# Optimization experiments

Hardware: AMD Instinct MI355X
Metric: run time of the kernel (lower is better)

Reference implementation:

```python
import jax, jax.numpy as jnp
import numpy as np

EPS = 1e-6

def _rmsnorm(x, w):
    # fp32 RMSNorm over last dim
    var = jnp.mean(x * x, axis=-1, keepdims=True)
    return w * (x * jax.lax.rsqrt(var + EPS))

def setup_inputs() -> dict:
    key = jax.random.key(0)
    ks = jax.random.split(key, 6)
    S, D, H = 4096, 1024, 16
    HD = D // H
    return {
        "hidden_states": jax.random.normal(ks[0], (S, D), jnp.float32),
        "qkv_w": jax.random.normal(ks[1], (3 * D, D), jnp.float32) * 0.02,
        "qkv_b": jnp.zeros((3 * D,), jnp.float32),
        "proj_w": jax.random.normal(ks[2], (D, D), jnp.float32) * 0.02,
        "proj_b": jnp.zeros((D,), jnp.float32),
        "q_norm_w": jnp.ones((D,), jnp.float32),
        "k_norm_w": jnp.ones((D,), jnp.float32),
        "rotary_freqs": jax.random.normal(ks[3], (S, HD // 2), jnp.float32),
        "cu_seqlens": jnp.array([0, 1024, 2048, 3072, 4096], jnp.int32),
        "num_heads": 16,
    }

def reference(hidden_states, qkv_w, qkv_b, proj_w, proj_b, q_norm_w, k_norm_w, rotary_freqs, cu_seqlens, num_heads):
    S, D = hidden_states.shape
    H = num_heads
    hd = D // H
    # QKV projection
    qkv = hidden_states @ qkv_w.T + qkv_b           # [S, 3D]
    qkv = qkv.reshape(S, 3, H, hd)
    q, k, v = qkv[:, 0], qkv[:, 1], qkv[:, 2]       # each [S, H, hd]
    # QK RMSNorm over the flattened hidden dim (InternVL style)
    q = _rmsnorm(q.reshape(S, D), q_norm_w).reshape(S, H, hd)
    k = _rmsnorm(k.reshape(S, D), k_norm_w).reshape(S, H, hd)
    # RoPE: freqs [S, hd/2] -> cos/sin [S, 1, hd] (tiled, not interleaved)
    cos = jnp.cos(rotary_freqs)
    sin = jnp.sin(rotary_freqs)
    cos = jnp.concatenate([cos, cos], axis=-1)[:, None, :]
    sin = jnp.concatenate([sin, sin], axis=-1)[:, None, :]
    def rope(t):
        x1, x2 = jnp.split(t, 2, axis=-1)
        rot = jnp.concatenate([-x2, x1], axis=-1)
        return t * cos + rot * sin
    q = rope(q)
    k = rope(k)
    # Block-diagonal mask from cu_seqlens: same-segment tokens attend
    seg = jnp.searchsorted(cu_seqlens[1:], jnp.arange(S), side='right')  # [S]
    mask = seg[:, None] == seg[None, :]                                   # [S, S]
    scale = 1.0 / jnp.sqrt(jnp.float32(hd))
    scores = jnp.einsum('shd,thd->hst', q, k) * scale                     # [H, S, S]
    scores = jnp.where(mask[None], scores, jnp.float32(-1e30))
    probs = jax.nn.softmax(scores, axis=-1)
    out = jnp.einsum('hst,thd->shd', probs, v).reshape(S, D)
    return out @ proj_w.T + proj_b
```

## Files before the change

kernel.cpp:

```cpp
#include <hip/hip_runtime.h>
#include <hip/hip_bf16.h>

#define S 4096
#define D 1024
#define NH 16
#define HD 64

typedef float f32x4 __attribute__((ext_vector_type(4)));
typedef __bf16 bf16x8 __attribute__((ext_vector_type(8)));

#define MFMA16(a, b, c) __builtin_amdgcn_mfma_f32_16x16x32_bf16((a), (b), (c), 0, 0, 0)

__device__ __forceinline__ unsigned short f2bf(float f) {
  unsigned int u = __builtin_bit_cast(unsigned int, f);
  u += 0x7FFFu + ((u >> 16) & 1u);
  return (unsigned short)(u >> 16);
}

__device__ __forceinline__ float bf2f(unsigned short u) {
  unsigned int x = ((unsigned int)u) << 16;
  return __builtin_bit_cast(float, x);
}

__device__ __forceinline__ unsigned cvtpk(float lo, float hi) {
  unsigned r;
  asm("v_cvt_pk_bf16_f32 %0, %1, %2" : "=v"(r) : "v"(lo), "v"(hi));
  return r;
}

typedef __attribute__((address_space(1))) void GAS;
typedef __attribute__((address_space(3))) void LAS;

__device__ __forceinline__ void gld_lds16(const unsigned short* g, unsigned short* l) {
  __builtin_amdgcn_global_load_lds((GAS*)g, (LAS*)l, 16, 0, 0);
}

__global__ void cvt3(const float* __restrict__ a, unsigned short* __restrict__ ao,
                     const float* __restrict__ b, unsigned short* __restrict__ bo,
                     const float* __restrict__ c, unsigned short* __restrict__ co) {
  int i = blockIdx.x * blockDim.x + threadIdx.x;
  const float* in;
  unsigned short* out;
  int j;
  if (i < 1048576) { in = a; out = ao; j = i; }
  else if (i < 1835008) { in = b; out = bo; j = i - 1048576; }
  else { in = c; out = co; j = i - 1835008; }
  float4 v = ((const float4*)in)[j];
  ushort4 u;
  u.x = f2bf(v.x); u.y = f2bf(v.y); u.z = f2bf(v.z); u.w = f2bf(v.w);
  ((ushort4*)out)[j] = u;
}

__device__ __forceinline__ int xcd_swz(int bid, int nwg) {
  int q = nwg >> 3;
  return (bid & 7) * q + (bid >> 3);
}

#define GSTEP(RA, RB, SA, SB, KN, COND)                                           \
  {                                                                               \
    bf16x8 af[4], bfv[4];                                                         \
    _Pragma("unroll") for (int mf = 0; mf < 4; ++mf)                              \
        af[mf] = *(const bf16x8*)&RA[(wr * 64 + mf * 16 + l15) * 32 + l4 * 8];    \
    _Pragma("unroll") for (int nf = 0; nf < 4; ++nf)                              \
        bfv[nf] = *(const bf16x8*)&RB[(wc * 64 + nf * 16 + l15) * 32 + l4 * 8];   \
    if (COND) {                                                                   \
      gld_lds16(Ab + (size_t)r0 * K + (KN) + o0, &SA[w * 512]);                   \
      gld_lds16(Ab + (size_t)r1 * K + (KN) + o1, &SA[2048 + w * 512]);            \
      gld_lds16(Bb + (size_t)r0 * K + (KN) + o0, &SB[w * 512]);                   \
      gld_lds16(Bb + (size_t)r1 * K + (KN) + o1, &SB[2048 + w * 512]);            \
    }                                                                             \
    _Pragma("unroll") for (int mf = 0; mf < 4; ++mf)                              \
        _Pragma("unroll") for (int nf = 0; nf < 4; ++nf)                          \
            acc[mf][nf] = MFMA16(af[mf], bfv[nf], acc[mf][nf]);                   \
    __syncthreads();                                                              \
  }

__global__ __launch_bounds__(256) void gemm_qkv(const unsigned short* __restrict__ A,
                                                const unsigned short* __restrict__ B,
                                                const float* __restrict__ bias,
                                                unsigned short* __restrict__ qk,
                                                unsigned short* __restrict__ vt) {
  __shared__ __align__(16) unsigned short As0[4096], As1[4096];
  __shared__ __align__(16) unsigned short Bs0[4096], Bs1[4096];
  __shared__ __align__(16) unsigned short tr[128 * 65];
  const int K = 1024;
  const int t = threadIdx.x;
  const int lane = t & 63;
  const int w = t >> 6;
  const int wr = w >> 1, wc = w & 1;
  const int l15 = lane & 15, l4 = lane >> 4;
  const int bid = blockIdx.y * 24 + blockIdx.x;
  const int r8 = bid & 7, i = bid >> 3;
  const int by = (r8 >> 1) * 8 + i / 12;
  const int bx = (r8 & 1) * 12 + i % 12;
  const int m0 = by * 128, n0 = bx * 128;

  f32x4 acc[4][4] = {};

  const int r0 = t >> 2, o0 = (t & 3) * 8;
  const int r1 = (256 + t) >> 2, o1 = ((256 + t) & 3) * 8;
  const unsigned short* Ab = A + (size_t)m0 * K;
  const unsigned short* Bb = B + (size_t)n0 * K;

  gld_lds16(Ab + (size_t)r0 * K + o0, &As0[w * 512]);
  gld_lds16(Ab + (size_t)r1 * K + o1, &As0[2048 + w * 512]);
  gld_lds16(Bb + (size_t)r0 * K + o0, &Bs0[w * 512]);
  gld_lds16(Bb + (size_t)r1 * K + o1, &Bs0[2048 + w * 512]);
  __syncthreads();

#pragma unroll 1
  for (int k0 = 0; k0 < K; k0 += 64) {
    GSTEP(As0, Bs0, As1, Bs1, k0 + 32, true);
    GSTEP(As1, Bs1, As0, Bs0, k0 + 64, k0 + 64 < K);
  }

  if (n0 < 2048) {
#pragma unroll
    for (int mf = 0; mf < 4; ++mf)
#pragma unroll
      for (int nf = 0; nf < 4; ++nf) {
        int rr = m0 + wr * 64 + mf * 16 + l4 * 4;
        int cc = n0 + wc * 64 + nf * 16 + l15;
        float bv = bias[cc];
#pragma unroll
        for (int j = 0; j < 4; ++j)
          qk[(size_t)(rr + j) * 2048 + cc] = f2bf(acc[mf][nf][j] + bv);
      }
  } else {
    const int h0 = (n0 - 2048) >> 6;
#pragma unroll
    for (int p = 0; p < 2; ++p) {
      if (wc == p) {
#pragma unroll
        for (int mf = 0; mf < 4; ++mf)
#pragma unroll
          for (int nf = 0; nf < 4; ++nf) {
            int srow = wr * 64 + mf * 16 + l4 * 4;
            int cl = nf * 16 + l15;
            float bv = bias[n0 + p * 64 + cl];
#pragma unroll
            for (int j = 0; j < 4; ++j)
              tr[(srow + j) * 65 + cl] = f2bf(acc[mf][nf][j] + bv);
          }
      }
      __syncthreads();
      const int hh = h0 + p;
#pragma unroll
      for (int i2 = 0; i2 < 8; ++i2) {
        int idx = i2 * 256 + t;
        int d = idx >> 5, sc = idx & 31;
        ushort4 u;
        u.x = tr[(sc * 4 + 0) * 65 + d];
        u.y = tr[(sc * 4 + 1) * 65 + d];
        u.z = tr[(sc * 4 + 2) * 65 + d];
        u.w = tr[(sc * 4 + 3) * 65 + d];
        *(ushort4*)(vt + (size_t)hh * HD * S + (size_t)d * S + m0 + sc * 4) = u;
      }
      __syncthreads();
    }
  }
}

__global__ __launch_bounds__(256) void gemm_bt(const unsigned short* __restrict__ A,
                                               const unsigned short* __restrict__ B,
                                               const float* __restrict__ bias,
                                               float* __restrict__ C,
                                               int M, int N, int K, int gx) {
  __shared__ __align__(16) unsigned short As0[4096], As1[4096];
  __shared__ __align__(16) unsigned short Bs0[4096], Bs1[4096];
  const int t = threadIdx.x;
  const int lane = t & 63;
  const int w = t >> 6;
  const int wr = w >> 1, wc = w & 1;
  const int l15 = lane & 15, l4 = lane >> 4;
  const int nwg = gridDim.x * gridDim.y;
  const int nbid = xcd_swz(blockIdx.y * gx + blockIdx.x, nwg);
  const int m0 = (nbid / gx) * 128, n0 = (nbid % gx) * 128;

  f32x4 acc[4][4] = {};

  const int r0 = t >> 2, o0 = (t & 3) * 8;
  const int r1 = (256 + t) >> 2, o1 = ((256 + t) & 3) * 8;
  const unsigned short* Ab = A + (size_t)m0 * K;
  const unsigned short* Bb = B + (size_t)n0 * K;

  gld_lds16(Ab + (size_t)r0 * K + o0, &As0[w * 512]);
  gld_lds16(Ab + (size_t)r1 * K + o1, &As0[2048 + w * 512]);
  gld_lds16(Bb + (size_t)r0 * K + o0, &Bs0[w * 512]);
  gld_lds16(Bb + (size_t)r1 * K + o1, &Bs0[2048 + w * 512]);
  __syncthreads();

#pragma unroll 1
  for (int k0 = 0; k0 < K; k0 += 64) {
    GSTEP(As0, Bs0, As1, Bs1, k0 + 32, true);
    GSTEP(As1, Bs1, As0, Bs0, k0 + 64, k0 + 64 < K);
  }

#pragma unroll
  for (int mf = 0; mf < 4; ++mf) {
#pragma unroll
    for (int nf = 0; nf < 4; ++nf) {
      int rr = m0 + wr * 64 + mf * 16 + l4 * 4;
      int cc = n0 + wc * 64 + nf * 16 + l15;
      float bv = bias[cc];
#pragma unroll
      for (int j = 0; j < 4; ++j)
        C[(size_t)(rr + j) * N + cc] = acc[mf][nf][j] + bv;
    }
  }
}

__global__ __launch_bounds__(256) void norm_rope(const unsigned short* __restrict__ qk,
                                                 const float* __restrict__ qw,
                                                 const float* __restrict__ kw,
                                                 const float* __restrict__ fr,
                                                 unsigned short* __restrict__ qo,
                                                 unsigned short* __restrict__ ko) {
  __shared__ float buf[1024];
  __shared__ float red[4];
  const int s = blockIdx.x, t = threadIdx.x;
  const int lane = t & 63, w = t >> 6;
  const int e = t * 4;
  const int hh = e >> 6, dd = e & 63;
  const float* frow = fr + (size_t)s * 32;
  float cs[4], sn[4];
#pragma unroll
  for (int i = 0; i < 4; ++i) {
    float f = frow[(dd + i) & 31];
    cs[i] = cosf(f);
    sn[i] = sinf(f);
  }
  for (int part = 0; part < 2; ++part) {
    const unsigned short* row = qk + (size_t)s * 2048 + part * 1024;
    const float* wvp = part ? kw : qw;
    unsigned short* op = part ? ko : qo;
    const float oscale = part ? 1.0f : 0.18033688011112042f;
    ushort4 uv = *(const ushort4*)(row + e);
    float vx = bf2f(uv.x), vy = bf2f(uv.y), vz = bf2f(uv.z), vw = bf2f(uv.w);
    float ssq = vx * vx + vy * vy + vz * vz + vw * vw;
#pragma unroll
    for (int off = 1; off < 64; off <<= 1) ssq += __shfl_xor(ssq, off, 64);
    if (part) __syncthreads();
    if (lane == 0) red[w] = ssq;
    __syncthreads();
    float inv = rsqrtf((red[0] + red[1] + red[2] + red[3]) * (1.0f / 1024.0f) + 1e-6f);
    float4 wv = *(const float4*)(wvp + e);
    buf[e + 0] = vx * inv * wv.x;
    buf[e + 1] = vy * inv * wv.y;
    buf[e + 2] = vz * inv * wv.z;
    buf[e + 3] = vw * inv * wv.w;
    __syncthreads();
    unsigned short ov[4];
#pragma unroll
    for (int i = 0; i < 4; ++i) {
      int di = dd + i;
      float x = buf[e + i];
      float rot = (di < 32) ? -buf[e + i + 32] : buf[e + i - 32];
      ov[i] = f2bf((x * cs[i] + rot * sn[i]) * oscale);
    }
    unsigned short* dst = op + (size_t)hh * S * HD + (size_t)s * HD + dd;
    dst[0] = ov[0]; dst[1] = ov[1]; dst[2] = ov[2]; dst[3] = ov[3];
  }
}

__device__ __forceinline__ void qk_tile(f32x4* s4, const unsigned short* Kbuf,
                                        bf16x8 qf0, bf16x8 qf1, int l15, int l4) {
#pragma unroll
  for (int nf = 0; nf < 4; ++nf) {
    const int row = nf * 16 + l15;
    const int roff = row * 64;
    const int sw = (row & 7) << 3;
    bf16x8 k0 = *(const bf16x8*)&Kbuf[roff + ((l4 * 8) ^ sw)];
    bf16x8 k1 = *(const bf16x8*)&Kbuf[roff + ((32 + l4 * 8) ^ sw)];
    s4[nf] = MFMA16(k0, qf0, s4[nf]);
    s4[nf] = MFMA16(k1, qf1, s4[nf]);
  }
}

__global__ __launch_bounds__(256) void attn_kernel(const unsigned short* __restrict__ q,
                                                   const unsigned short* __restrict__ k,
                                                   const unsigned short* __restrict__ vt,
                                                   unsigned short* __restrict__ aout) {
  __shared__ __align__(16) unsigned short Ks[2][4096];
  __shared__ __align__(16) unsigned short Vs[3][4096];
  const int bid = blockIdx.x;
  const int xcd = bid & 7;
  const int idx = bid >> 3;
  const int gw = idx >> 4, qt = idx & 15;
  const int g = xcd * 8 + gw;
  const int h = g >> 2, seg = g & 3;
  const int t = threadIdx.x, lane = t & 63, w = t >> 6;
  const int l15 = lane & 15, l4 = lane >> 4;
  const size_t hb = (size_t)h * S * HD;
  const int q0 = seg * 1024 + qt * 64 + w * 16;
  const int kvbase = seg * 1024;

  const int sr = t >> 3;
  const int scb = (t & 7) ^ (sr & 7);
  const unsigned short* ksrcA = k + hb + (size_t)(kvbase + sr) * HD + scb * 8;
  const unsigned short* ksrcB = ksrcA + 32 * HD;
  const unsigned short* vsrcA = vt + (size_t)h * HD * S + (size_t)sr * S + kvbase + scb * 8;
  const unsigned short* vsrcB = vsrcA + (size_t)32 * S;

  const unsigned short* qp = q + hb + (size_t)(q0 + l15) * HD + l4 * 8;
  bf16x8 qf0 = *(const bf16x8*)qp;
  bf16x8 qf1 = *(const bf16x8*)(qp + 32);

  f32x4 o[4] = {};
  float m = -1e30f, l = 0.f;

  gld_lds16(ksrcA, &Ks[0][w * 512]);
  gld_lds16(ksrcB, &Ks[0][2048 + w * 512]);
  gld_lds16(ksrcA + 4096, &Ks[1][w * 512]);
  gld_lds16(ksrcB + 4096, &Ks[1][2048 + w * 512]);
  gld_lds16(vsrcA, &Vs[0][w * 512]);
  gld_lds16(vsrcB, &Vs[0][2048 + w * 512]);
  gld_lds16(vsrcA + 64, &Vs[1][w * 512]);
  gld_lds16(vsrcB + 64, &Vs[1][2048 + w * 512]);
  __syncthreads();

  f32x4 cur[4] = {};
  qk_tile(cur, Ks[0], qf0, qf1, l15, l4);
  __syncthreads();

#pragma unroll
  for (int it = 0; it < 16; ++it) {
    if (it < 14) {
      gld_lds16(ksrcA + (it + 2) * 4096, &Ks[it & 1][w * 512]);
      gld_lds16(ksrcB + (it + 2) * 4096, &Ks[it & 1][2048 + w * 512]);
      gld_lds16(vsrcA + (it + 2) * 64, &Vs[(it + 2) % 3][w * 512]);
      gld_lds16(vsrcB + (it + 2) * 64, &Vs[(it + 2) % 3][2048 + w * 512]);
    }
    f32x4 nxt[4] = {};
    if (it < 15) {
      __builtin_amdgcn_s_setprio(1);
      qk_tile(nxt, Ks[(it + 1) & 1], qf0, qf1, l15, l4);
      __builtin_amdgcn_s_setprio(0);
      __builtin_amdgcn_sched_barrier(0);
    }
    float t0 = fmaxf(fmaxf(cur[0][0], cur[0][1]), cur[0][2]);
    float t1 = fmaxf(fmaxf(cur[0][3], cur[1][0]), cur[1][1]);
    float t2 = fmaxf(fmaxf(cur[1][2], cur[1][3]), cur[2][0]);
    float t3 = fmaxf(fmaxf(cur[2][1], cur[2][2]), cur[2][3]);
    float t4 = fmaxf(fmaxf(cur[3][0], cur[3][1]), cur[3][2]);
    float lmax = fmaxf(fmaxf(fmaxf(t0, t1), fmaxf(t2, t3)), fmaxf(t4, cur[3][3]));
    if (!__all(lmax <= m + 8.0f)) {
      float tmax = fmaxf(lmax, __shfl_xor(lmax, 16, 64));
      tmax = fmaxf(tmax, __shfl_xor(tmax, 32, 64));
      const float mn = fmaxf(m, tmax);
      const float corr = exp2f(m - mn);
      m = mn;
      l *= corr;
#pragma unroll
      for (int nf2 = 0; nf2 < 4; ++nf2)
#pragma unroll
        for (int j = 0; j < 4; ++j) o[nf2][j] *= corr;
    }
    float p[4][4];
#pragma unroll
    for (int nf = 0; nf < 4; ++nf)
#pragma unroll
      for (int j = 0; j < 4; ++j) {
        float e = exp2f(cur[nf][j] - m);
        p[nf][j] = e;
        l += e;
      }
    unsigned pk[4][2];
#pragma unroll
    for (int nf = 0; nf < 4; ++nf) {
      pk[nf][0] = cvtpk(p[nf][0], p[nf][1]);
      pk[nf][1] = cvtpk(p[nf][2], p[nf][3]);
    }
    const int srcbase = ((lane >> 4) & 1) * 32 + l15;
    const bool hi = (lane & 32) != 0;
    const unsigned short* Vbuf = Vs[it % 3];
#pragma unroll
    for (int ks = 0; ks < 2; ++ks) {
      unsigned bw[4];
#pragma unroll
      for (int h2 = 0; h2 < 2; ++h2)
#pragma unroll
        for (int r = 0; r < 2; ++r) {
          unsigned E = (unsigned)__shfl((int)pk[2 * ks][r], srcbase + h2 * 16, 64);
          unsigned F = (unsigned)__shfl((int)pk[2 * ks + 1][r], srcbase + h2 * 16, 64);
          bw[h2 * 2 + r] = hi ? F : E;
        }
      bf16x8 pb = __builtin_bit_cast(bf16x8, *(uint4*)bw);
      __builtin_amdgcn_s_setprio(1);
#pragma unroll
      for (int nf2 = 0; nf2 < 4; ++nf2) {
        const int row = nf2 * 16 + l15;
        const int roff = row * 64;
        const int sw = (row & 7) << 3;
        bf16x8 vf = *(const bf16x8*)&Vbuf[roff + ((ks * 32 + l4 * 8) ^ sw)];
        o[nf2] = MFMA16(vf, pb, o[nf2]);
      }
      __builtin_amdgcn_s_setprio(0);
    }
    __syncthreads();
    cur[0] = nxt[0]; cur[1] = nxt[1]; cur[2] = nxt[2]; cur[3] = nxt[3];
  }

  l += __shfl_xor(l, 16, 64);
  l += __shfl_xor(l, 32, 64);
  const float invl = 1.0f / l;
#pragma unroll
  for (int nf2 = 0; nf2 < 4; ++nf2) {
    ushort4 u;
    u.x = f2bf(o[nf2][0] * invl);
    u.y = f2bf(o[nf2][1] * invl);
    u.z = f2bf(o[nf2][2] * invl);
    u.w = f2bf(o[nf2][3] * invl);
    *(ushort4*)(aout + (size_t)(q0 + l15) * D + h * 64 + nf2 * 16 + l4 * 4) = u;
  }
}

extern "C" void kernel_launch(void* const* d_in, const int* in_sizes, int n_in,
                              void* d_out, int out_size, void* d_ws, size_t ws_size,
                              hipStream_t stream) {
  const float* hidden = (const float*)d_in[0];
  const float* qkvw   = (const float*)d_in[1];
  const float* qkvb   = (const float*)d_in[2];
  const float* projw  = (const float*)d_in[3];
  const float* projb  = (const float*)d_in[4];
  const float* qnw    = (const float*)d_in[5];
  const float* knw    = (const float*)d_in[6];
  const float* freqs  = (const float*)d_in[7];
  float* out = (float*)d_out;
  char* ws = (char*)d_ws;

  unsigned short* hb  = (unsigned short*)(ws + 0);
  unsigned short* wb  = (unsigned short*)(ws + (8u << 20));
  unsigned short* pb  = (unsigned short*)(ws + (14u << 20));
  unsigned short* qk  = (unsigned short*)(ws + (16u << 20));
  unsigned short* vtb = (unsigned short*)(ws + (32u << 20));
  unsigned short* qb  = (unsigned short*)(ws + (40u << 20));
  unsigned short* kb  = (unsigned short*)(ws + (48u << 20));
  unsigned short* ab  = (unsigned short*)(ws + (56u << 20));

  cvt3<<<8192, 256, 0, stream>>>(hidden, hb, qkvw, wb, projw, pb);
  gemm_qkv<<<dim3(24, 32), 256, 0, stream>>>(hb, wb, qkvb, qk, vtb);
  norm_rope<<<4096, 256, 0, stream>>>(qk, qnw, knw, freqs, qb, kb);
  attn_kernel<<<1024, 256, 0, stream>>>(qb, kb, vtb, ab);
  gemm_bt<<<dim3(8, 32), 256, 0, stream>>>(ab, pb, projb, out, 4096, 1024, 1024, 8);
}
```

Before: 133.4 us.

## Process two 16-row query groups per wave in attention to reuse K/V tiles

Each wave now handles 32 query rows (two 16-row groups) instead of 16. Each K and V fragment read from LDS feeds two MFMAs, and each block covers 128 queries, so the grid drops from 1024 to 512 blocks. This halves global K/V tile loads and LDS fragment reads per query. The cost is more accumulator and score registers, which may lower occupancy, and fewer blocks to spread across CUs.

```diff
diff --git a/kernel.cpp b/kernel.cpp
--- a/kernel.cpp
+++ b/kernel.cpp
@@ -263,8 +263,9 @@
   }
 }
 
-__device__ __forceinline__ void qk_tile(f32x4* s4, const unsigned short* Kbuf,
-                                        bf16x8 qf0, bf16x8 qf1, int l15, int l4) {
+__device__ __forceinline__ void qk_tile2(f32x4* sA, f32x4* sB, const unsigned short* Kbuf,
+                                         bf16x8 qA0, bf16x8 qA1, bf16x8 qB0, bf16x8 qB1,
+                                         int l15, int l4) {
 #pragma unroll
   for (int nf = 0; nf < 4; ++nf) {
     const int row = nf * 16 + l15;
@@ -272,8 +273,10 @@
     const int sw = (row & 7) << 3;
     bf16x8 k0 = *(const bf16x8*)&Kbuf[roff + ((l4 * 8) ^ sw)];
     bf16x8 k1 = *(const bf16x8*)&Kbuf[roff + ((32 + l4 * 8) ^ sw)];
-    s4[nf] = MFMA16(k0, qf0, s4[nf]);
-    s4[nf] = MFMA16(k1, qf1, s4[nf]);
+    sA[nf] = MFMA16(k0, qA0, sA[nf]);
+    sA[nf] = MFMA16(k1, qA1, sA[nf]);
+    sB[nf] = MFMA16(k0, qB0, sB[nf]);
+    sB[nf] = MFMA16(k1, qB1, sB[nf]);
   }
 }
 
@@ -286,13 +289,13 @@
   const int bid = blockIdx.x;
   const int xcd = bid & 7;
   const int idx = bid >> 3;
-  const int gw = idx >> 4, qt = idx & 15;
+  const int gw = idx >> 3, qt = idx & 7;
   const int g = xcd * 8 + gw;
   const int h = g >> 2, seg = g & 3;
   const int t = threadIdx.x, lane = t & 63, w = t >> 6;
   const int l15 = lane & 15, l4 = lane >> 4;
   const size_t hb = (size_t)h * S * HD;
-  const int q0 = seg * 1024 + qt * 64 + w * 16;
+  const int q0 = seg * 1024 + qt * 128 + w * 32;
   const int kvbase = seg * 1024;
 
   const int sr = t >> 3;
@@ -302,12 +305,15 @@
   const unsigned short* vsrcA = vt + (size_t)h * HD * S + (size_t)sr * S + kvbase + scb * 8;
   const unsigned short* vsrcB = vsrcA + (size_t)32 * S;
 
-  const unsigned short* qp = q + hb + (size_t)(q0 + l15) * HD + l4 * 8;
-  bf16x8 qf0 = *(const bf16x8*)qp;
-  bf16x8 qf1 = *(const bf16x8*)(qp + 32);
-
-  f32x4 o[4] = {};
-  float m = -1e30f, l = 0.f;
+  const unsigned short* qpA = q + hb + (size_t)(q0 + l15) * HD + l4 * 8;
+  const unsigned short* qpB = q + hb + (size_t)(q0 + 16 + l15) * HD + l4 * 8;
+  bf16x8 qA0 = *(const bf16x8*)qpA;
+  bf16x8 qA1 = *(const bf16x8*)(qpA + 32);
+  bf16x8 qB0 = *(const bf16x8*)qpB;
+  bf16x8 qB1 = *(const bf16x8*)(qpB + 32);
+
+  f32x4 oA[4] = {}, oB[4] = {};
+  float mA = -1e30f, lA = 0.f, mB = -1e30f, lB = 0.f;
 
   gld_lds16(ksrcA, &Ks[0][w * 512]);
   gld_lds16(ksrcB, &Ks[0][2048 + w * 512]);
@@ -319,8 +325,8 @@
   gld_lds16(vsrcB + 64, &Vs[1][2048 + w * 512]);
   __syncthreads();
 
-  f32x4 cur[4] = {};
-  qk_tile(cur, Ks[0], qf0, qf1, l15, l4);
+  f32x4 curA[4] = {}, curB[4] = {};
+  qk_tile2(curA, curB, Ks[0], qA0, qA1, qB0, qB1, l15, l4);
   __syncthreads();
 
 #pragma unroll
@@ -331,61 +337,73 @@
       gld_lds16(vsrcA + (it + 2) * 64, &Vs[(it + 2) % 3][w * 512]);
       gld_lds16(vsrcB + (it + 2) * 64, &Vs[(it + 2) % 3][2048 + w * 512]);
     }
-    f32x4 nxt[4] = {};
+    f32x4 nxtA[4] = {}, nxtB[4] = {};
     if (it < 15) {
       __builtin_amdgcn_s_setprio(1);
-      qk_tile(nxt, Ks[(it + 1) & 1], qf0, qf1, l15, l4);
+      qk_tile2(nxtA, nxtB, Ks[(it + 1) & 1], qA0, qA1, qB0, qB1, l15, l4);
       __builtin_amdgcn_s_setprio(0);
       __builtin_amdgcn_sched_barrier(0);
     }
-    float t0 = fmaxf(fmaxf(cur[0][0], cur[0][1]), cur[0][2]);
-    float t1 = fmaxf(fmaxf(cur[0][3], cur[1][0]), cur[1][1]);
-    float t2 = fmaxf(fmaxf(cur[1][2], cur[1][3]), cur[2][0]);
-    float t3 = fmaxf(fmaxf(cur[2][1], cur[2][2]), cur[2][3]);
-    float t4 = fmaxf(fmaxf(cur[3][0], cur[3][1]), cur[3][2]);
-    float lmax = fmaxf(fmaxf(fmaxf(t0, t1), fmaxf(t2, t3)), fmaxf(t4, cur[3][3]));
-    if (!__all(lmax <= m + 8.0f)) {
-      float tmax = fmaxf(lmax, __shfl_xor(lmax, 16, 64));
-      tmax = fmaxf(tmax, __shfl_xor(tmax, 32, 64));
-      const float mn = fmaxf(m, tmax);
-      const float corr = exp2f(m - mn);
-      m = mn;
-      l *= corr;
-#pragma unroll
-      for (int nf2 = 0; nf2 < 4; ++nf2)
-#pragma unroll
-        for (int j = 0; j < 4; ++j) o[nf2][j] *= corr;
-    }
-    float p[4][4];
-#pragma unroll
-    for (int nf = 0; nf < 4; ++nf)
-#pragma unroll
-      for (int j = 0; j < 4; ++j) {
-        float e = exp2f(cur[nf][j] - m);
-        p[nf][j] = e;
-        l += e;
-      }
-    unsigned pk[4][2];
-#pragma unroll
-    for (int nf = 0; nf < 4; ++nf) {
-      pk[nf][0] = cvtpk(p[nf][0], p[nf][1]);
-      pk[nf][1] = cvtpk(p[nf][2], p[nf][3]);
+    unsigned pkA[4][2], pkB[4][2];
+#pragma unroll
+    for (int gq = 0; gq < 2; ++gq) {
+      f32x4* cur = gq ? curB : curA;
+      float& m = gq ? mB : mA;
+      float& l = gq ? lB : lA;
+      f32x4* o = gq ? oB : oA;
+      unsigned(*pk)[2] = gq ? pkB : pkA;
+      float t0 = fmaxf(fmaxf(cur[0][0], cur[0][1]), cur[0][2]);
+      float t1 = fmaxf(fmaxf(cur[0][3], cur[1][0]), cur[1][1]);
+      float t2 = fmaxf(fmaxf(cur[1][2], cur[1][3]), cur[2][0]);
+      float t3 = fmaxf(fmaxf(cur[2][1], cur[2][2]), cur[2][3]);
+      float t4 = fmaxf(fmaxf(cur[3][0], cur[3][1]), cur[3][2]);
+      float lmax = fmaxf(fmaxf(fmaxf(t0, t1), fmaxf(t2, t3)), fmaxf(t4, cur[3][3]));
+      if (!__all(lmax <= m + 8.0f)) {
+        float tmax = fmaxf(lmax, __shfl_xor(lmax, 16, 64));
+        tmax = fmaxf(tmax, __shfl_xor(tmax, 32, 64));
+        const float mn = fmaxf(m, tmax);
+        const float corr = exp2f(m - mn);
+        m = mn;
+        l *= corr;
+#pragma unroll
+        for (int nf2 = 0; nf2 < 4; ++nf2)
+#pragma unroll
+          for (int j = 0; j < 4; ++j) o[nf2][j] *= corr;
+      }
+      float p[4][4];
+#pragma unroll
+      for (int nf = 0; nf < 4; ++nf)
+#pragma unroll
+        for (int j = 0; j < 4; ++j) {
+          float e = exp2f(cur[nf][j] - m);
+          p[nf][j] = e;
+          l += e;
+        }
+#pragma unroll
+      for (int nf = 0; nf < 4; ++nf) {
+        pk[nf][0] = cvtpk(p[nf][0], p[nf][1]);
+        pk[nf][1] = cvtpk(p[nf][2], p[nf][3]);
+      }
     }
     const int srcbase = ((lane >> 4) & 1) * 32 + l15;
     const bool hi = (lane & 32) != 0;
     const unsigned short* Vbuf = Vs[it % 3];
 #pragma unroll
     for (int ks = 0; ks < 2; ++ks) {
-      unsigned bw[4];
+      unsigned bwA[4], bwB[4];
 #pragma unroll
       for (int h2 = 0; h2 < 2; ++h2)
 #pragma unroll
         for (int r = 0; r < 2; ++r) {
-          unsigned E = (unsigned)__shfl((int)pk[2 * ks][r], srcbase + h2 * 16, 64);
-          unsigned F = (unsigned)__shfl((int)pk[2 * ks + 1][r], srcbase + h2 * 16, 64);
-          bw[h2 * 2 + r] = hi ? F : E;
+          unsigned EA = (unsigned)__shfl((int)pkA[2 * ks][r], srcbase + h2 * 16, 64);
+          unsigned FA = (unsigned)__shfl((int)pkA[2 * ks + 1][r], srcbase + h2 * 16, 64);
+          bwA[h2 * 2 + r] = hi ? FA : EA;
+          unsigned EB = (unsigned)__shfl((int)pkB[2 * ks][r], srcbase + h2 * 16, 64);
+          unsigned FB = (unsigned)__shfl((int)pkB[2 * ks + 1][r], srcbase + h2 * 16, 64);
+          bwB[h2 * 2 + r] = hi ? FB : EB;
         }
-      bf16x8 pb = __builtin_bit_cast(bf16x8, *(uint4*)bw);
+      bf16x8 pbA = __builtin_bit_cast(bf16x8, *(uint4*)bwA);
+      bf16x8 pbB = __builtin_bit_cast(bf16x8, *(uint4*)bwB);
       __builtin_amdgcn_s_setprio(1);
 #pragma unroll
       for (int nf2 = 0; nf2 < 4; ++nf2) {
@@ -393,25 +411,35 @@
         const int roff = row * 64;
         const int sw = (row & 7) << 3;
         bf16x8 vf = *(const bf16x8*)&Vbuf[roff + ((ks * 32 + l4 * 8) ^ sw)];
-        o[nf2] = MFMA16(vf, pb, o[nf2]);
+        oA[nf2] = MFMA16(vf, pbA, oA[nf2]);
+        oB[nf2] = MFMA16(vf, pbB, oB[nf2]);
       }
       __builtin_amdgcn_s_setprio(0);
     }
     __syncthreads();
-    cur[0] = nxt[0]; cur[1] = nxt[1]; cur[2] = nxt[2]; cur[3] = nxt[3];
-  }
-
-  l += __shfl_xor(l, 16, 64);
-  l += __shfl_xor(l, 32, 64);
-  const float invl = 1.0f / l;
+#pragma unroll
+    for (int nf = 0; nf < 4; ++nf) { curA[nf] = nxtA[nf]; curB[nf] = nxtB[nf]; }
+  }
+
+  lA += __shfl_xor(lA, 16, 64);
+  lA += __shfl_xor(lA, 32, 64);
+  lB += __shfl_xor(lB, 16, 64);
+  lB += __shfl_xor(lB, 32, 64);
+  const float invA = 1.0f / lA, invB = 1.0f / lB;
 #pragma unroll
   for (int nf2 = 0; nf2 < 4; ++nf2) {
     ushort4 u;
-    u.x = f2bf(o[nf2][0] * invl);
-    u.y = f2bf(o[nf2][1] * invl);
-    u.z = f2bf(o[nf2][2] * invl);
-    u.w = f2bf(o[nf2][3] * invl);
+    u.x = f2bf(oA[nf2][0] * invA);
+    u.y = f2bf(oA[nf2][1] * invA);
+    u.z = f2bf(oA[nf2][2] * invA);
+    u.w = f2bf(oA[nf2][3] * invA);
     *(ushort4*)(aout + (size_t)(q0 + l15) * D + h * 64 + nf2 * 16 + l4 * 4) = u;
+    ushort4 v;
+    v.x = f2bf(oB[nf2][0] * invB);
+    v.y = f2bf(oB[nf2][1] * invB);
+    v.z = f2bf(oB[nf2][2] * invB);
+    v.w = f2bf(oB[nf2][3] * invB);
+    *(ushort4*)(aout + (size_t)(q0 + 16 + l15) * D + h * 64 + nf2 * 16 + l4 * 4) = v;
   }
 }
 
@@ -441,6 +469,6 @@
   cvt3<<<8192, 256, 0, stream>>>(hidden, hb, qkvw, wb, projw, pb);
   gemm_qkv<<<dim3(24, 32), 256, 0, stream>>>(hb, wb, qkvb, qk, vtb);
   norm_rope<<<4096, 256, 0, stream>>>(qk, qnw, knw, freqs, qb, kb);
-  attn_kernel<<<1024, 256, 0, stream>>>(qb, kb, vtb, ab);
+  attn_kernel<<<512, 256, 0, stream>>>(qb, kb, vtb, ab);
   gemm_bt<<<dim3(8, 32), 256, 0, stream>>>(ab, pb, projb, out, 4096, 1024, 1024, 8);
 }
```

Measured after the change: 136.0 us. Within noise of the previous version (+2.0%).

## Triple-buffer GEMM LDS stages with explicit vmcnt waits and raw barriers

Applied to the files above, without the earlier changes.

Replaces the double-buffered GEMM main loop in both the QKV and output-projection kernels with a three-stage LDS ring. Two K-slices are prefetched up front, and each step issues the next load, runs its MFMAs, then waits only for the older load group (vmcnt(4)) before a raw s_barrier instead of __syncthreads. This lets global-to-LDS loads run one stage further ahead of compute, at the cost of 50% more LDS for the operand buffers, which may lower occupancy. K is hardcoded to 1024, and a barrier is moved ahead of each V-transpose write so the tr buffer reuse stays safe.

```diff
diff --git a/kernel.cpp b/kernel.cpp
--- a/kernel.cpp
+++ b/kernel.cpp
@@ -56,34 +56,77 @@
   return (bid & 7) * q + (bid >> 3);
 }
 
-#define GSTEP(RA, RB, SA, SB, KN, COND)                                           \
-  {                                                                               \
-    bf16x8 af[4], bfv[4];                                                         \
-    _Pragma("unroll") for (int mf = 0; mf < 4; ++mf)                              \
-        af[mf] = *(const bf16x8*)&RA[(wr * 64 + mf * 16 + l15) * 32 + l4 * 8];    \
-    _Pragma("unroll") for (int nf = 0; nf < 4; ++nf)                              \
-        bfv[nf] = *(const bf16x8*)&RB[(wc * 64 + nf * 16 + l15) * 32 + l4 * 8];   \
-    if (COND) {                                                                   \
-      gld_lds16(Ab + (size_t)r0 * K + (KN) + o0, &SA[w * 512]);                   \
-      gld_lds16(Ab + (size_t)r1 * K + (KN) + o1, &SA[2048 + w * 512]);            \
-      gld_lds16(Bb + (size_t)r0 * K + (KN) + o0, &SB[w * 512]);                   \
-      gld_lds16(Bb + (size_t)r1 * K + (KN) + o1, &SB[2048 + w * 512]);            \
-    }                                                                             \
-    _Pragma("unroll") for (int mf = 0; mf < 4; ++mf)                              \
-        _Pragma("unroll") for (int nf = 0; nf < 4; ++nf)                          \
-            acc[mf][nf] = MFMA16(af[mf], bfv[nf], acc[mf][nf]);                   \
-    __syncthreads();                                                              \
-  }
+#define DSTEP_S(RA, RB, SA, SB, KN, VM)                                          \
+  {                                                                              \
+    bf16x8 af[4], bfv[4];                                                        \
+    _Pragma("unroll") for (int mf = 0; mf < 4; ++mf)                             \
+        af[mf] = *(const bf16x8*)&RA[(wr * 64 + mf * 16 + l15) * 32 + l4 * 8];   \
+    _Pragma("unroll") for (int nf = 0; nf < 4; ++nf)                             \
+        bfv[nf] = *(const bf16x8*)&RB[(wc * 64 + nf * 16 + l15) * 32 + l4 * 8];  \
+    gld_lds16(Ab + (size_t)r0 * 1024 + (KN) + o0, &SA[w * 512]);                 \
+    gld_lds16(Ab + (size_t)r1 * 1024 + (KN) + o1, &SA[2048 + w * 512]);          \
+    gld_lds16(Bb + (size_t)r0 * 1024 + (KN) + o0, &SB[w * 512]);                 \
+    gld_lds16(Bb + (size_t)r1 * 1024 + (KN) + o1, &SB[2048 + w * 512]);          \
+    _Pragma("unroll") for (int mf = 0; mf < 4; ++mf)                             \
+        _Pragma("unroll") for (int nf = 0; nf < 4; ++nf)                         \
+            acc[mf][nf] = MFMA16(af[mf], bfv[nf], acc[mf][nf]);                  \
+    asm volatile("s_waitcnt vmcnt(" VM ")" ::: "memory");                        \
+    __builtin_amdgcn_s_barrier();                                                \
+  }
+
+#define DSTEP_N(RA, RB, VM)                                                      \
+  {                                                                              \
+    bf16x8 af[4], bfv[4];                                                        \
+    _Pragma("unroll") for (int mf = 0; mf < 4; ++mf)                             \
+        af[mf] = *(const bf16x8*)&RA[(wr * 64 + mf * 16 + l15) * 32 + l4 * 8];   \
+    _Pragma("unroll") for (int nf = 0; nf < 4; ++nf)                             \
+        bfv[nf] = *(const bf16x8*)&RB[(wc * 64 + nf * 16 + l15) * 32 + l4 * 8];  \
+    _Pragma("unroll") for (int mf = 0; mf < 4; ++mf)                             \
+        _Pragma("unroll") for (int nf = 0; nf < 4; ++nf)                         \
+            acc[mf][nf] = MFMA16(af[mf], bfv[nf], acc[mf][nf]);                  \
+    asm volatile("s_waitcnt vmcnt(" VM ")" ::: "memory");                        \
+    __builtin_amdgcn_s_barrier();                                                \
+  }
+
+#define DSTEP_LAST(RA, RB)                                                       \
+  {                                                                              \
+    bf16x8 af[4], bfv[4];                                                        \
+    _Pragma("unroll") for (int mf = 0; mf < 4; ++mf)                             \
+        af[mf] = *(const bf16x8*)&RA[(wr * 64 + mf * 16 + l15) * 32 + l4 * 8];   \
+    _Pragma("unroll") for (int nf = 0; nf < 4; ++nf)                             \
+        bfv[nf] = *(const bf16x8*)&RB[(wc * 64 + nf * 16 + l15) * 32 + l4 * 8];  \
+    _Pragma("unroll") for (int mf = 0; mf < 4; ++mf)                             \
+        _Pragma("unroll") for (int nf = 0; nf < 4; ++nf)                         \
+            acc[mf][nf] = MFMA16(af[mf], bfv[nf], acc[mf][nf]);                  \
+  }
+
+#define GEMM_PRO_LOOP()                                                          \
+  gld_lds16(Ab + (size_t)r0 * 1024 + o0, &As0[w * 512]);                         \
+  gld_lds16(Ab + (size_t)r1 * 1024 + o1, &As0[2048 + w * 512]);                  \
+  gld_lds16(Bb + (size_t)r0 * 1024 + o0, &Bs0[w * 512]);                         \
+  gld_lds16(Bb + (size_t)r1 * 1024 + o1, &Bs0[2048 + w * 512]);                  \
+  gld_lds16(Ab + (size_t)r0 * 1024 + 32 + o0, &As1[w * 512]);                    \
+  gld_lds16(Ab + (size_t)r1 * 1024 + 32 + o1, &As1[2048 + w * 512]);             \
+  gld_lds16(Bb + (size_t)r0 * 1024 + 32 + o0, &Bs1[w * 512]);                    \
+  gld_lds16(Bb + (size_t)r1 * 1024 + 32 + o1, &Bs1[2048 + w * 512]);             \
+  asm volatile("s_waitcnt vmcnt(4)" ::: "memory");                               \
+  __builtin_amdgcn_s_barrier();                                                  \
+  _Pragma("unroll 1") for (int k0 = 0; k0 < 960; k0 += 96) {                     \
+    DSTEP_S(As0, Bs0, As2, Bs2, k0 + 64, "4")                                    \
+    DSTEP_S(As1, Bs1, As0, Bs0, k0 + 96, "4")                                    \
+    DSTEP_S(As2, Bs2, As1, Bs1, k0 + 128, "4")                                   \
+  }                                                                              \
+  DSTEP_N(As0, Bs0, "0")                                                         \
+  DSTEP_LAST(As1, Bs1)
 
 __global__ __launch_bounds__(256) void gemm_qkv(const unsigned short* __restrict__ A,
                                                 const unsigned short* __restrict__ B,
                                                 const float* __restrict__ bias,
                                                 unsigned short* __restrict__ qk,
                                                 unsigned short* __restrict__ vt) {
-  __shared__ __align__(16) unsigned short As0[4096], As1[4096];
-  __shared__ __align__(16) unsigned short Bs0[4096], Bs1[4096];
+  __shared__ __align__(16) unsigned short As0[4096], As1[4096], As2[4096];
+  __shared__ __align__(16) unsigned short Bs0[4096], Bs1[4096], Bs2[4096];
   __shared__ __align__(16) unsigned short tr[128 * 65];
-  const int K = 1024;
   const int t = threadIdx.x;
   const int lane = t & 63;
   const int w = t >> 6;
@@ -99,20 +142,10 @@
 
   const int r0 = t >> 2, o0 = (t & 3) * 8;
   const int r1 = (256 + t) >> 2, o1 = ((256 + t) & 3) * 8;
-  const unsigned short* Ab = A + (size_t)m0 * K;
-  const unsigned short* Bb = B + (size_t)n0 * K;
-
-  gld_lds16(Ab + (size_t)r0 * K + o0, &As0[w * 512]);
-  gld_lds16(Ab + (size_t)r1 * K + o1, &As0[2048 + w * 512]);
-  gld_lds16(Bb + (size_t)r0 * K + o0, &Bs0[w * 512]);
-  gld_lds16(Bb + (size_t)r1 * K + o1, &Bs0[2048 + w * 512]);
-  __syncthreads();
-
-#pragma unroll 1
-  for (int k0 = 0; k0 < K; k0 += 64) {
-    GSTEP(As0, Bs0, As1, Bs1, k0 + 32, true);
-    GSTEP(As1, Bs1, As0, Bs0, k0 + 64, k0 + 64 < K);
-  }
+  const unsigned short* Ab = A + (size_t)m0 * 1024;
+  const unsigned short* Bb = B + (size_t)n0 * 1024;
+
+  GEMM_PRO_LOOP()
 
   if (n0 < 2048) {
 #pragma unroll
@@ -130,6 +163,7 @@
     const int h0 = (n0 - 2048) >> 6;
 #pragma unroll
     for (int p = 0; p < 2; ++p) {
+      __syncthreads();
       if (wc == p) {
 #pragma unroll
         for (int mf = 0; mf < 4; ++mf)
@@ -156,7 +190,6 @@
         u.w = tr[(sc * 4 + 3) * 65 + d];
         *(ushort4*)(vt + (size_t)hh * HD * S + (size_t)d * S + m0 + sc * 4) = u;
       }
-      __syncthreads();
     }
   }
 }
@@ -166,8 +199,8 @@
                                                const float* __restrict__ bias,
                                                float* __restrict__ C,
                                                int M, int N, int K, int gx) {
-  __shared__ __align__(16) unsigned short As0[4096], As1[4096];
-  __shared__ __align__(16) unsigned short Bs0[4096], Bs1[4096];
+  __shared__ __align__(16) unsigned short As0[4096], As1[4096], As2[4096];
+  __shared__ __align__(16) unsigned short Bs0[4096], Bs1[4096], Bs2[4096];
   const int t = threadIdx.x;
   const int lane = t & 63;
   const int w = t >> 6;
@@ -181,20 +214,10 @@
 
   const int r0 = t >> 2, o0 = (t & 3) * 8;
   const int r1 = (256 + t) >> 2, o1 = ((256 + t) & 3) * 8;
-  const unsigned short* Ab = A + (size_t)m0 * K;
-  const unsigned short* Bb = B + (size_t)n0 * K;
-
-  gld_lds16(Ab + (size_t)r0 * K + o0, &As0[w * 512]);
-  gld_lds16(Ab + (size_t)r1 * K + o1, &As0[2048 + w * 512]);
-  gld_lds16(Bb + (size_t)r0 * K + o0, &Bs0[w * 512]);
-  gld_lds16(Bb + (size_t)r1 * K + o1, &Bs0[2048 + w * 512]);
-  __syncthreads();
-
-#pragma unroll 1
-  for (int k0 = 0; k0 < K; k0 += 64) {
-    GSTEP(As0, Bs0, As1, Bs1, k0 + 32, true);
-    GSTEP(As1, Bs1, As0, Bs0, k0 + 64, k0 + 64 < K);
-  }
+  const unsigned short* Ab = A + (size_t)m0 * 1024;
+  const unsigned short* Bb = B + (size_t)n0 * 1024;
+
+  GEMM_PRO_LOOP()
 
 #pragma unroll
   for (int mf = 0; mf < 4; ++mf) {
```

Measured after the change: 126.4 us. 1.06x faster.
